# Performance work log

Hardware: AMD Instinct MI355X
Metric: run time of the kernel (lower is better)

The kernel has to match this reference:

```python
import jax, jax.numpy as jnp
import numpy as np

B = 65536
BASE_CW = 0.5  # constraint weight at epoch 0 (progress=0)

def setup_inputs() -> dict:
    key = jax.random.key(0)
    k1, k2 = jax.random.split(key)
    outputs = jax.random.normal(k1, (B, 81, 9), dtype=jnp.float32)
    targets = jax.random.randint(k2, (B, 81), 0, 9, dtype=jnp.int64)
    return {"outputs": outputs, "targets": targets}

def reference(outputs, targets):
    b = outputs.shape[0]
    # log-softmax over the 9 digit classes (single stable pass)
    logp = jax.nn.log_softmax(outputs, axis=2)            # (B, 81, 9)
    t = targets.reshape(-1)                               # (B*81,)
    # cross entropy (mean over all cells)
    ce = -jnp.take_along_axis(logp.reshape(-1, 9), t[:, None], axis=1).mean()
    probs = jnp.exp(logp)                                 # softmax probs
    grid = probs.reshape(b, 9, 9, 9)                      # (B, row, col, digit)
    # all 27 constraint MSEs fused: per-digit mean over (B, 9), summed over digits
    row_sums = grid.sum(axis=2)                           # (B, 9, 9)
    col_sums = grid.sum(axis=1)                           # (B, 9, 9)
    box_sums = grid.reshape(b, 3, 3, 3, 3, 9).sum(axis=(2, 4)).reshape(b, 9, 9)
    constraint_loss = (
        jnp.mean((row_sums - 1.0) ** 2, axis=(0, 1)).sum()
        + jnp.mean((col_sums - 1.0) ** 2, axis=(0, 1)).sum()
        + jnp.mean((box_sums - 1.0) ** 2, axis=(0, 1)).sum()
    ) / 27.0
    # confidence (entropy) term, masked by targets != -1
    mask = (t != -1).astype(outputs.dtype)                # (B*81,)
    conf = -(probs.reshape(-1, 9) * logp.reshape(-1, 9)).sum(axis=1)
    conf = (conf * mask).sum() / (mask.sum() + 1e-8)
    return ce + BASE_CW * constraint_loss + 0.1 * conf
```

## Files before the change

### kernel.cpp

```cpp
#include <hip/hip_runtime.h>
#include <stdint.h>

#define THREADS 256
#define BPB 8
#define NVEC  (BPB * 729 / 4)
#define NBLK  (65536 / BPB)
#define NUNIT (27 * BPB)

__launch_bounds__(THREADS)
static __global__ void sudoku_main(const float* __restrict__ outs,
                                   const int*   __restrict__ targets,
                                   float*       __restrict__ partials) {
    __shared__ __align__(16) float L[BPB * 729];
    __shared__ float wave_sums[THREADS / 64];

    const int tid  = threadIdx.x;
    const int lane = tid & 63;
    const int wv   = tid >> 6;
    const long long board0 = (long long)blockIdx.x * BPB;
    const float* __restrict__ gsrc = outs + board0 * 729;

    #pragma unroll
    for (int k = 0; k < 6; ++k) {
        const int vbase = k * THREADS + wv * 64;
        const int idx   = vbase + lane;
        if (idx < NVEC) {
            __builtin_amdgcn_global_load_lds(
                (const __attribute__((address_space(1))) void*)(gsrc + (size_t)idx * 4),
                (__attribute__((address_space(3))) void*)(&L[vbase * 4]),
                16, 0, 0);
        }
    }
    __syncthreads();

    float acc_a = 0.0f;
    float acc_c = 0.0f;
    if (tid < NUNIT) {
        const int b    = tid & 7;
        const int u27  = tid >> 3;
        const int type = u27 / 9;
        const int unit = u27 - type * 9;
        const int ur3  = (unit / 3) * 3;
        const int uc3  = (unit % 3) * 3;
        const float* __restrict__ Lb = &L[b * 729];
        const int*   __restrict__ tb = targets + (board0 + b) * 81;

        float acc[9];
        #pragma unroll
        for (int d = 0; d < 9; ++d) acc[d] = 0.0f;

        #pragma unroll
        for (int k = 0; k < 9; ++k) {
            const int cbox = (ur3 + k / 3) * 9 + uc3 + (k % 3);
            const int c = (type == 0) ? (unit * 9 + k)
                        : ((type == 1) ? (k * 9 + unit) : cbox);
            const float* __restrict__ xp = Lb + c * 9;
            float x[9], e[9];
            #pragma unroll
            for (int i = 0; i < 9; ++i) x[i] = xp[i];
            float s = 0.0f, sx = 0.0f;
            #pragma unroll
            for (int i = 0; i < 9; ++i) {
                e[i] = __expf(x[i]);
                s += e[i];
                sx = fmaf(e[i], x[i], sx);
            }
            const float inv = __builtin_amdgcn_rcpf(s);
            #pragma unroll
            for (int i = 0; i < 9; ++i) acc[i] = fmaf(e[i], inv, acc[i]);

            if (type == 0) {
                const int t = tb[c];
                float xt = x[0];
                #pragma unroll
                for (int i = 1; i < 9; ++i) xt = (i == t) ? x[i] : xt;
                const float lse = __logf(s);
                acc_a += (lse - xt) + 0.1f * (lse - sx * inv);
            }
        }
        #pragma unroll
        for (int d = 0; d < 9; ++d) {
            const float dd = acc[d] - 1.0f;
            acc_c = fmaf(dd, dd, acc_c);
        }
    }

    const float SA = 1.0f / (65536.0f * 81.0f);
    const float SB = 0.5f / (27.0f * 65536.0f * 9.0f);
    float total = acc_a * SA + acc_c * SB;
    #pragma unroll
    for (int off = 32; off > 0; off >>= 1)
        total += __shfl_down(total, off, 64);
    if ((tid & 63) == 0) wave_sums[tid >> 6] = total;
    __syncthreads();
    if (tid == 0)
        partials[blockIdx.x] = wave_sums[0] + wave_sums[1] + wave_sums[2] + wave_sums[3];
}

__launch_bounds__(THREADS)
static __global__ void sudoku_final(const float* __restrict__ partials,
                                    float*       __restrict__ out) {
    __shared__ float wave_sums[THREADS / 64];
    const int tid = threadIdx.x;
    const float4* __restrict__ p4 = (const float4*)partials;
    float s = 0.0f;
    #pragma unroll 4
    for (int i = tid; i < NBLK / 4; i += THREADS) {
        const float4 v = p4[i];
        s += (v.x + v.y) + (v.z + v.w);
    }
    #pragma unroll
    for (int off = 32; off > 0; off >>= 1)
        s += __shfl_down(s, off, 64);
    if ((tid & 63) == 0) wave_sums[tid >> 6] = s;
    __syncthreads();
    if (tid == 0)
        out[0] = wave_sums[0] + wave_sums[1] + wave_sums[2] + wave_sums[3];
}

extern "C" void kernel_launch(void* const* d_in, const int* in_sizes, int n_in,
                              void* d_out, int out_size, void* d_ws, size_t ws_size,
                              hipStream_t stream) {
    const float* outs    = (const float*)d_in[0];
    const int*   targets = (const int*)d_in[1];
    float*       partials = (float*)d_ws;
    hipLaunchKernelGGL(sudoku_main, dim3(NBLK), dim3(THREADS), 0, stream,
                       outs, targets, partials);
    hipLaunchKernelGGL(sudoku_final, dim3(1), dim3(THREADS), 0, stream,
                       partials, (float*)d_out);
}
```

Before: 283.0 us.

## Compute softmax once per cell across all threads, then sum constraints from LDS

Previously each of 216 threads recomputed softmax for 9 cells of its row, column or box, so every cell was exponentiated three times and 40 threads sat idle. Now all 256 threads compute softmax, CE and entropy once per cell, write the probabilities back into LDS, and after a barrier a subset of threads sums row, column and box probabilities. The block size is halved to 4 boards, targets are loaded coalesced, and an occupancy hint is added to launch bounds. This adds an extra barrier and LDS write traffic in exchange for removing redundant exp work.

```diff
diff --git a/kernel.cpp b/kernel.cpp
--- a/kernel.cpp
+++ b/kernel.cpp
@@ -2,12 +2,12 @@
 #include <stdint.h>
 
 #define THREADS 256
-#define BPB 8
+#define BPB 4
+#define CELLS (BPB * 81)
 #define NVEC  (BPB * 729 / 4)
 #define NBLK  (65536 / BPB)
-#define NUNIT (27 * BPB)
 
-__launch_bounds__(THREADS)
+__launch_bounds__(THREADS, 8)
 static __global__ void sudoku_main(const float* __restrict__ outs,
                                    const int*   __restrict__ targets,
                                    float*       __restrict__ partials) {
@@ -19,9 +19,10 @@
     const int wv   = tid >> 6;
     const long long board0 = (long long)blockIdx.x * BPB;
     const float* __restrict__ gsrc = outs + board0 * 729;
+    const int*   __restrict__ tsrc = targets + board0 * 81;
 
     #pragma unroll
-    for (int k = 0; k < 6; ++k) {
+    for (int k = 0; k < 3; ++k) {
         const int vbase = k * THREADS + wv * 64;
         const int idx   = vbase + lane;
         if (idx < NVEC) {
@@ -31,30 +32,17 @@
                 16, 0, 0);
         }
     }
+    const int t0 = tsrc[tid];
+    const int t1 = (tid < CELLS - THREADS) ? tsrc[tid + THREADS] : 0;
     __syncthreads();
 
     float acc_a = 0.0f;
-    float acc_c = 0.0f;
-    if (tid < NUNIT) {
-        const int b    = tid & 7;
-        const int u27  = tid >> 3;
-        const int type = u27 / 9;
-        const int unit = u27 - type * 9;
-        const int ur3  = (unit / 3) * 3;
-        const int uc3  = (unit % 3) * 3;
-        const float* __restrict__ Lb = &L[b * 729];
-        const int*   __restrict__ tb = targets + (board0 + b) * 81;
-
-        float acc[9];
-        #pragma unroll
-        for (int d = 0; d < 9; ++d) acc[d] = 0.0f;
-
-        #pragma unroll
-        for (int k = 0; k < 9; ++k) {
-            const int cbox = (ur3 + k / 3) * 9 + uc3 + (k % 3);
-            const int c = (type == 0) ? (unit * 9 + k)
-                        : ((type == 1) ? (k * 9 + unit) : cbox);
-            const float* __restrict__ xp = Lb + c * 9;
+    #pragma unroll
+    for (int it = 0; it < 2; ++it) {
+        const int cell = tid + it * THREADS;
+        if (cell < CELLS) {
+            float* __restrict__ xp = &L[cell * 9];
+            const int t = (it == 0) ? t0 : t1;
             float x[9], e[9];
             #pragma unroll
             for (int i = 0; i < 9; ++i) x[i] = xp[i];
@@ -65,18 +53,40 @@
                 s += e[i];
                 sx = fmaf(e[i], x[i], sx);
             }
+            float xt = x[0];
+            #pragma unroll
+            for (int i = 1; i < 9; ++i) xt = (i == t) ? x[i] : xt;
+            const float lse = __logf(s);
             const float inv = __builtin_amdgcn_rcpf(s);
+            acc_a += (lse - xt) + 0.1f * (lse - sx * inv);
             #pragma unroll
-            for (int i = 0; i < 9; ++i) acc[i] = fmaf(e[i], inv, acc[i]);
+            for (int i = 0; i < 9; ++i) xp[i] = e[i] * inv;
+        }
+    }
+    __syncthreads();
 
-            if (type == 0) {
-                const int t = tb[c];
-                float xt = x[0];
-                #pragma unroll
-                for (int i = 1; i < 9; ++i) xt = (i == t) ? x[i] : xt;
-                const float lse = __logf(s);
-                acc_a += (lse - xt) + 0.1f * (lse - sx * inv);
-            }
+    float acc_c = 0.0f;
+    if (tid < 27 * BPB) {
+        const int q    = tid & 3;
+        const int u27  = tid >> 2;
+        const int type = u27 / 9;
+        const int unit = u27 - type * 9;
+        const int ur3  = (unit / 3) * 3;
+        const int uc3  = (unit % 3) * 3;
+        const float* __restrict__ Pq = &L[q * 729];
+
+        float acc[9];
+        #pragma unroll
+        for (int d = 0; d < 9; ++d) acc[d] = 0.0f;
+        #pragma unroll
+        for (int j = 0; j < 9; ++j) {
+            const int crow = unit * 9 + j;
+            const int ccol = j * 9 + unit;
+            const int cbox = (ur3 + j / 3) * 9 + uc3 + (j % 3);
+            const int c = (type == 0) ? crow : ((type == 1) ? ccol : cbox);
+            const float* __restrict__ cp = Pq + c * 9;
+            #pragma unroll
+            for (int d = 0; d < 9; ++d) acc[d] += cp[d];
         }
         #pragma unroll
         for (int d = 0; d < 9; ++d) {
```

Result: slower. 300.6 us (+6.2%).

## Use single-wave blocks of four boards and stage targets through LDS

Applied to the files above, without the earlier changes.

The main kernel now runs one 64-lane wavefront per block over four boards instead of four waves over eight boards. Each lane handles up to two constraint units, and the block barrier is replaced by a plain vmcnt wait. Targets are also copied into LDS with the async global-to-LDS load, and the target logit is picked by an indexed LDS read instead of a select chain. The aim is to remove block-level synchronisation and give the scheduler more, smaller blocks to overlap loads with compute. The cost is more blocks and partials, a second partially-idle unit iteration per lane, and dropping the launch bounds on the main kernel.

```diff
diff --git a/kernel.cpp b/kernel.cpp
--- a/kernel.cpp
+++ b/kernel.cpp
@@ -1,87 +1,93 @@
 #include <hip/hip_runtime.h>
 #include <stdint.h>
 
-#define THREADS 256
-#define BPB 8
-#define NVEC  (BPB * 729 / 4)
-#define NBLK  (65536 / BPB)
-#define NUNIT (27 * BPB)
+#define THREADS 64
+#define SPB 4
+#define NBLK (65536 / SPB)
+#define NUNIT (27 * SPB)
 
-__launch_bounds__(THREADS)
 static __global__ void sudoku_main(const float* __restrict__ outs,
                                    const int*   __restrict__ targets,
                                    float*       __restrict__ partials) {
-    __shared__ __align__(16) float L[BPB * 729];
-    __shared__ float wave_sums[THREADS / 64];
+    __shared__ __align__(16) float L[SPB * 729];
+    __shared__ __align__(16) int   T[SPB * 81];
 
-    const int tid  = threadIdx.x;
-    const int lane = tid & 63;
-    const int wv   = tid >> 6;
-    const long long board0 = (long long)blockIdx.x * BPB;
+    const int lane = threadIdx.x;
+    const long long board0 = (long long)blockIdx.x * SPB;
     const float* __restrict__ gsrc = outs + board0 * 729;
+    const int*   __restrict__ tsrc = targets + board0 * 81;
 
     #pragma unroll
-    for (int k = 0; k < 6; ++k) {
-        const int vbase = k * THREADS + wv * 64;
-        const int idx   = vbase + lane;
-        if (idx < NVEC) {
+    for (int k = 0; k < 12; ++k) {
+        const int idx = k * 64 + lane;
+        if (idx < 729) {
             __builtin_amdgcn_global_load_lds(
                 (const __attribute__((address_space(1))) void*)(gsrc + (size_t)idx * 4),
-                (__attribute__((address_space(3))) void*)(&L[vbase * 4]),
+                (__attribute__((address_space(3))) void*)(&L[k * 256]),
                 16, 0, 0);
         }
     }
-    __syncthreads();
+    #pragma unroll
+    for (int k = 0; k < 2; ++k) {
+        const int idx = k * 64 + lane;
+        if (idx < 81) {
+            __builtin_amdgcn_global_load_lds(
+                (const __attribute__((address_space(1))) void*)(tsrc + (size_t)idx * 4),
+                (__attribute__((address_space(3))) void*)(&T[k * 256]),
+                16, 0, 0);
+        }
+    }
+    asm volatile("s_waitcnt vmcnt(0)" ::: "memory");
 
-    float acc_a = 0.0f;
-    float acc_c = 0.0f;
-    if (tid < NUNIT) {
-        const int b    = tid & 7;
-        const int u27  = tid >> 3;
-        const int type = u27 / 9;
-        const int unit = u27 - type * 9;
-        const int ur3  = (unit / 3) * 3;
-        const int uc3  = (unit % 3) * 3;
-        const float* __restrict__ Lb = &L[b * 729];
-        const int*   __restrict__ tb = targets + (board0 + b) * 81;
+    float acc_a = 0.0f, acc_c = 0.0f;
+    #pragma unroll
+    for (int it = 0; it < 2; ++it) {
+        const int u = it * 64 + lane;
+        if (u < NUNIT) {
+            const int b    = u & 3;
+            const int u27  = u >> 2;
+            const int type = u27 / 9;
+            const int unit = u27 - type * 9;
+            const int ur3  = (unit / 3) * 3;
+            const int uc3  = (unit % 3) * 3;
+            const float* __restrict__ Lb = &L[b * 729];
+            const int*   __restrict__ Tb = &T[b * 81];
 
-        float acc[9];
-        #pragma unroll
-        for (int d = 0; d < 9; ++d) acc[d] = 0.0f;
+            float acc[9];
+            #pragma unroll
+            for (int d = 0; d < 9; ++d) acc[d] = 0.0f;
 
-        #pragma unroll
-        for (int k = 0; k < 9; ++k) {
-            const int cbox = (ur3 + k / 3) * 9 + uc3 + (k % 3);
-            const int c = (type == 0) ? (unit * 9 + k)
-                        : ((type == 1) ? (k * 9 + unit) : cbox);
-            const float* __restrict__ xp = Lb + c * 9;
-            float x[9], e[9];
             #pragma unroll
-            for (int i = 0; i < 9; ++i) x[i] = xp[i];
-            float s = 0.0f, sx = 0.0f;
+            for (int k = 0; k < 9; ++k) {
+                const int cbox = (ur3 + k / 3) * 9 + uc3 + (k % 3);
+                const int c = (type == 0) ? (unit * 9 + k)
+                            : ((type == 1) ? (k * 9 + unit) : cbox);
+                const float* __restrict__ xp = Lb + c * 9;
+                float x[9], e[9];
+                #pragma unroll
+                for (int i = 0; i < 9; ++i) x[i] = xp[i];
+                float s = 0.0f, sx = 0.0f;
+                #pragma unroll
+                for (int i = 0; i < 9; ++i) {
+                    e[i] = __expf(x[i]);
+                    s += e[i];
+                    sx = fmaf(e[i], x[i], sx);
+                }
+                const float inv = __builtin_amdgcn_rcpf(s);
+                #pragma unroll
+                for (int i = 0; i < 9; ++i) acc[i] = fmaf(e[i], inv, acc[i]);
+
+                if (type == 0) {
+                    const float xt  = xp[Tb[c]];
+                    const float lse = __logf(s);
+                    acc_a += (lse - xt) + 0.1f * (lse - sx * inv);
+                }
+            }
             #pragma unroll
-            for (int i = 0; i < 9; ++i) {
-                e[i] = __expf(x[i]);
-                s += e[i];
-                sx = fmaf(e[i], x[i], sx);
+            for (int d = 0; d < 9; ++d) {
+                const float dd = acc[d] - 1.0f;
+                acc_c = fmaf(dd, dd, acc_c);
             }
-            const float inv = __builtin_amdgcn_rcpf(s);
-            #pragma unroll
-            for (int i = 0; i < 9; ++i) acc[i] = fmaf(e[i], inv, acc[i]);
-
-            if (type == 0) {
-                const int t = tb[c];
-                float xt = x[0];
-                #pragma unroll
-                for (int i = 1; i < 9; ++i) xt = (i == t) ? x[i] : xt;
-                const float lse = __logf(s);
-                acc_a += (lse - xt) + 0.1f * (lse - sx * inv);
-            }
-        }
-        #pragma unroll
-        for (int d = 0; d < 9; ++d) {
-            const float dd = acc[d] - 1.0f;
-            acc_c = fmaf(dd, dd, acc_c);
         }
     }
 
@@ -91,21 +97,19 @@
     #pragma unroll
     for (int off = 32; off > 0; off >>= 1)
         total += __shfl_down(total, off, 64);
-    if ((tid & 63) == 0) wave_sums[tid >> 6] = total;
-    __syncthreads();
-    if (tid == 0)
-        partials[blockIdx.x] = wave_sums[0] + wave_sums[1] + wave_sums[2] + wave_sums[3];
+    if (lane == 0)
+        partials[blockIdx.x] = total;
 }
 
-__launch_bounds__(THREADS)
+__launch_bounds__(256)
 static __global__ void sudoku_final(const float* __restrict__ partials,
                                     float*       __restrict__ out) {
-    __shared__ float wave_sums[THREADS / 64];
+    __shared__ float wave_sums[4];
     const int tid = threadIdx.x;
     const float4* __restrict__ p4 = (const float4*)partials;
     float s = 0.0f;
     #pragma unroll 4
-    for (int i = tid; i < NBLK / 4; i += THREADS) {
+    for (int i = tid; i < NBLK / 4; i += 256) {
         const float4 v = p4[i];
         s += (v.x + v.y) + (v.z + v.w);
     }
@@ -126,6 +130,6 @@
     float*       partials = (float*)d_ws;
     hipLaunchKernelGGL(sudoku_main, dim3(NBLK), dim3(THREADS), 0, stream,
                        outs, targets, partials);
-    hipLaunchKernelGGL(sudoku_final, dim3(1), dim3(THREADS), 0, stream,
+    hipLaunchKernelGGL(sudoku_final, dim3(1), dim3(256), 0, stream,
                        partials, (float*)d_out);
 }
```

After: 281.3 us. Within noise of the previous version (-0.6%).
